# Kernel optimization log

Hardware: AMD Instinct MI355X
Metric: run time of the kernel (lower is better)

## Reference

```python
import jax, jax.numpy as jnp
import numpy as np

N_NODES = 50000
N_EDGES = 800000
IN_DIM = 128
HID = 128
N_LAYERS = 2


def setup_inputs() -> dict:
    key = jax.random.key(0)
    ks = jax.random.split(key, 16)
    x = jax.random.normal(ks[0], (N_NODES, IN_DIM), dtype=jnp.float32)
    edge_index = jax.random.randint(ks[1], (2, N_EDGES), 0, N_NODES, dtype=jnp.int64)
    def lin(k, fan_in, fan_out):
        bound = 1.0 / np.sqrt(fan_in)
        k1, k2 = jax.random.split(k)
        W = jax.random.uniform(k1, (fan_in, fan_out), jnp.float32, -bound, bound)
        b = jax.random.uniform(k2, (fan_out,), jnp.float32, -bound, bound)
        return W, b
    W1_0, b1_0 = lin(ks[2], IN_DIM, HID)
    W2_0, b2_0 = lin(ks[3], HID, HID)
    W1_1, b1_1 = lin(ks[4], HID, HID)
    W2_1, b2_1 = lin(ks[5], HID, HID)
    Wr, br = lin(ks[6], HID, 1)
    return dict(x=x, edge_index=edge_index,
                W1_0=W1_0, b1_0=b1_0, W2_0=W2_0, b2_0=b2_0,
                W1_1=W1_1, b1_1=b1_1, W2_1=W2_1, b2_1=b2_1,
                Wr=Wr, br=br)


def _gin_conv(x, src, dst, W1, b1, W2, b2):
    # GINConv (eps=0): h = MLP(x + sum_{j in N(i)} x_j)
    msgs = x[src]                                   # [E, d] gather
    agg = jax.ops.segment_sum(msgs, dst, num_segments=x.shape[0])  # [N, d] scatter-add
    h = x + agg
    h = jax.nn.relu(h @ W1 + b1)
    return h @ W2 + b2


def reference(x, edge_index, W1_0, b1_0, W2_0, b2_0, W1_1, b1_1, W2_1, b2_1, Wr, br):
    src, dst = edge_index[0], edge_index[1]
    # layer 0
    h = jax.nn.relu(_gin_conv(x, src, dst, W1_0, b1_0, W2_0, b2_0))
    # layer 1 (dropout is identity in eval mode)
    h = jax.nn.relu(_gin_conv(h, src, dst, W1_1, b1_1, W2_1, b2_1))
    return h @ Wr + br
```

## Files before the change

kernel.cpp:

```cpp
#include <hip/hip_runtime.h>

#define HIDDEN 128
#define NB_SHIFT 7
#define NPB 128
#define EPB 4096

typedef __attribute__((ext_vector_type(8))) short short8;
typedef __attribute__((ext_vector_type(4))) float f32x4;
typedef _Float16 f16;
typedef __attribute__((ext_vector_type(8))) _Float16 f16x8;

__device__ __forceinline__ ushort f2bf(float a) {
  union { float f; unsigned u; } c; c.f = a;
  return (ushort)((c.u + 0x7FFFu + ((c.u >> 16) & 1u)) >> 16);
}
__device__ __forceinline__ float bf2f(ushort h) {
  union { unsigned u; float f; } c; c.u = ((unsigned)h) << 16;
  return c.f;
}

__global__ __launch_bounds__(256) void bucket_hist_kernel(
    const int* __restrict__ dst, int* __restrict__ bcnt, int E, int NB) {
  __shared__ int loc[512];
  const int t = threadIdx.x;
  loc[t] = 0; loc[t + 256] = 0;
  __syncthreads();
  const int base = blockIdx.x * EPB;
  const int end = min(base + EPB, E);
  for (int e = base + t; e < end; e += 256)
    atomicAdd(&loc[dst[e] >> NB_SHIFT], 1);
  __syncthreads();
  for (int b = t; b < NB; b += 256)
    if (loc[b]) atomicAdd(&bcnt[b], loc[b]);
}

__global__ __launch_bounds__(256) void scan_buckets_kernel(
    const int* __restrict__ bcnt, int* __restrict__ pairOff,
    int* __restrict__ gCursor, int NB) {
  __shared__ int sh[512];
  const int t = threadIdx.x;
  const int v0 = (t < NB) ? bcnt[t] : 0;
  const int v1 = (t + 256 < NB) ? bcnt[t + 256] : 0;
  sh[t] = v0; sh[t + 256] = v1;
  __syncthreads();
#pragma unroll
  for (int off = 1; off < 512; off <<= 1) {
    int a = (t >= off) ? sh[t - off] : 0;
    int b = (t + 256 >= off) ? sh[t + 256 - off] : 0;
    __syncthreads();
    sh[t] += a; sh[t + 256] += b;
    __syncthreads();
  }
  const int e0 = sh[t] - v0;
  const int e1 = sh[t + 256] - v1;
  pairOff[t] = e0; gCursor[t] = e0;
  pairOff[t + 256] = e1; gCursor[t + 256] = e1;
  if (t == 255) pairOff[512] = sh[511];
}

__global__ __launch_bounds__(256) void partition_kernel(
    const int* __restrict__ src, const int* __restrict__ dst,
    int* __restrict__ gCursor, int* __restrict__ pairs, int E, int NB) {
  __shared__ int loc[512];
  __shared__ int cur[512];
  const int t = threadIdx.x;
  loc[t] = 0; loc[t + 256] = 0;
  __syncthreads();
  const int base = blockIdx.x * EPB;
  const int end = min(base + EPB, E);
  for (int e = base + t; e < end; e += 256)
    atomicAdd(&loc[dst[e] >> NB_SHIFT], 1);
  __syncthreads();
  for (int b = t; b < NB; b += 256)
    cur[b] = loc[b] ? atomicAdd(&gCursor[b], loc[b]) : 0;
  __syncthreads();
  for (int e = base + t; e < end; e += 256) {
    const int d = dst[e];
    const int p = atomicAdd(&cur[d >> NB_SHIFT], 1);
    pairs[p] = ((d & (NPB - 1)) << 25) | src[e];
  }
}

__global__ __launch_bounds__(256) void build_csr_kernel(
    const int* __restrict__ pairs, const int* __restrict__ pairOff,
    int* __restrict__ rowptr, int* __restrict__ col, int M, int E, int NB) {
  __shared__ int deg[NPB];
  __shared__ int pre[NPB];
  __shared__ int cur[NPB];
  const int b = blockIdx.x;
  const int t = threadIdx.x;
  const int s = pairOff[b];
  const int e2 = pairOff[b + 1];
  const int nodeBase = b << NB_SHIFT;
  const int nNodes = min(NPB, M - nodeBase);
  if (t < NPB) deg[t] = 0;
  __syncthreads();
  for (int i = s + t; i < e2; i += 256)
    atomicAdd(&deg[((unsigned)pairs[i]) >> 25], 1);
  __syncthreads();
  if (t < NPB) pre[t] = deg[t];
  __syncthreads();
#pragma unroll
  for (int off = 1; off < NPB; off <<= 1) {
    int v = (t < NPB && t >= off) ? pre[t - off] : 0;
    __syncthreads();
    if (t < NPB) pre[t] += v;
    __syncthreads();
  }
  if (t < nNodes) rowptr[nodeBase + t] = s + pre[t] - deg[t];
  if (b == NB - 1 && t == 0) rowptr[M] = E;
  if (t < NPB) cur[t] = pre[t] - deg[t];
  __syncthreads();
  for (int i = s + t; i < e2; i += 256) {
    const int pr = pairs[i];
    const int pos = s + atomicAdd(&cur[((unsigned)pr) >> 25], 1);
    col[pos] = pr & 0x1FFFFFF;
  }
}

__global__ __launch_bounds__(256) void f2h_kernel(const float* __restrict__ in,
                                                  f16* __restrict__ out, int n8) {
  int i = blockIdx.x * 256 + threadIdx.x;
  if (i >= n8) return;
  const float4* p = (const float4*)(in + (size_t)i * 8);
  float4 a = p[0], b = p[1];
  f16x8 o;
  o[0] = (f16)a.x; o[1] = (f16)a.y; o[2] = (f16)a.z; o[3] = (f16)a.w;
  o[4] = (f16)b.x; o[5] = (f16)b.y; o[6] = (f16)b.z; o[7] = (f16)b.w;
  *(f16x8*)(out + (size_t)i * 8) = o;
}

__global__ __launch_bounds__(256) void prepack_kernel(
    const float* __restrict__ Wa, const float* __restrict__ Wb,
    const float* __restrict__ Wc, const float* __restrict__ Wd,
    ushort* __restrict__ out) {
  int idx = blockIdx.x * 256 + threadIdx.x;
  int w = idx >> 11;
  int rem = idx & 2047;
  int ks = rem >> 9;
  int nf = (rem >> 6) & 7;
  int lane = rem & 63;
  const float* W = (w == 0) ? Wa : (w == 1) ? Wb : (w == 2) ? Wc : Wd;
  const int kbase = ks * 32 + (lane >> 4) * 8;
  const int n = nf * 16 + (lane & 15);
  ushort* oh = out + (size_t)w * 32768 + (size_t)rem * 8;
  ushort* ol = oh + 16384;
#pragma unroll
  for (int j = 0; j < 8; ++j) {
    float v = W[(size_t)(kbase + j) * HIDDEN + n];
    ushort h = f2bf(v);
    oh[j] = h;
    ol[j] = f2bf(v - bf2f(h));
  }
}

__global__ __launch_bounds__(256, 4) void gin_layer_kernel(
    const f16* __restrict__ xh, const int* __restrict__ rowptr,
    const int* __restrict__ col, const ushort* __restrict__ W1p,
    const float* __restrict__ b1, const ushort* __restrict__ W2p,
    const float* __restrict__ b2, f16* __restrict__ Ch,
    const float* __restrict__ Wr, const float* __restrict__ br,
    float* __restrict__ outv, int M, int doReadout) {
  __shared__ float h1[4][16][132];
  const int t = threadIdx.x;
  const int lane = t & 63;
  const int w = t >> 6;
  const int r = lane & 15;
  const int g = lane >> 4;
  const int mBase = blockIdx.x * 64 + w * 16;
  int arow = mBase + r;
  if (arow > M - 1) arow = M - 1;

  float a32[4][8];
  {
    const f16* rp = xh + (size_t)arow * HIDDEN + g * 8;
    f16x8 s0 = *(const f16x8*)(rp);
    f16x8 s1 = *(const f16x8*)(rp + 32);
    f16x8 s2 = *(const f16x8*)(rp + 64);
    f16x8 s3 = *(const f16x8*)(rp + 96);
#pragma unroll
    for (int j = 0; j < 8; ++j) {
      a32[0][j] = (float)s0[j]; a32[1][j] = (float)s1[j];
      a32[2][j] = (float)s2[j]; a32[3][j] = (float)s3[j];
    }
    const int s = rowptr[arow];
    const int e = rowptr[arow + 1];
    int i = s;
    for (; i + 1 < e; i += 2) {
      const int c0 = col[i], c1 = col[i + 1];
      const f16* p0 = xh + (size_t)c0 * HIDDEN + g * 8;
      const f16* p1 = xh + (size_t)c1 * HIDDEN + g * 8;
      f16x8 u0 = *(const f16x8*)(p0);
      f16x8 u1 = *(const f16x8*)(p0 + 32);
      f16x8 u2 = *(const f16x8*)(p0 + 64);
      f16x8 u3 = *(const f16x8*)(p0 + 96);
      f16x8 v0 = *(const f16x8*)(p1);
      f16x8 v1 = *(const f16x8*)(p1 + 32);
      f16x8 v2 = *(const f16x8*)(p1 + 64);
      f16x8 v3 = *(const f16x8*)(p1 + 96);
#pragma unroll
      for (int j = 0; j < 8; ++j) {
        a32[0][j] += (float)u0[j] + (float)v0[j];
        a32[1][j] += (float)u1[j] + (float)v1[j];
        a32[2][j] += (float)u2[j] + (float)v2[j];
        a32[3][j] += (float)u3[j] + (float)v3[j];
      }
    }
    if (i < e) {
      const int c0 = col[i];
      const f16* p0 = xh + (size_t)c0 * HIDDEN + g * 8;
      f16x8 u0 = *(const f16x8*)(p0);
      f16x8 u1 = *(const f16x8*)(p0 + 32);
      f16x8 u2 = *(const f16x8*)(p0 + 64);
      f16x8 u3 = *(const f16x8*)(p0 + 96);
#pragma unroll
      for (int j = 0; j < 8; ++j) {
        a32[0][j] += (float)u0[j];
        a32[1][j] += (float)u1[j];
        a32[2][j] += (float)u2[j];
        a32[3][j] += (float)u3[j];
      }
    }
  }

  f32x4 acc[8];
#pragma unroll
  for (int i = 0; i < 8; ++i) acc[i] = (f32x4){0.f, 0.f, 0.f, 0.f};

#pragma unroll
  for (int ks = 0; ks < 4; ++ks) {
    short8 ah, al;
#pragma unroll
    for (int j = 0; j < 8; ++j) {
      ushort h = f2bf(a32[ks][j]);
      ah[j] = (short)h;
      al[j] = (short)f2bf(a32[ks][j] - bf2f(h));
    }
#pragma unroll
    for (int nf = 0; nf < 8; ++nf) {
      const ushort* bp = W1p + ((size_t)(ks * 8 + nf) * 64 + lane) * 8;
      short8 bh = *(const short8*)bp;
      short8 bl = *(const short8*)(bp + 16384);
      acc[nf] = __builtin_amdgcn_mfma_f32_16x16x32_bf16(ah, bh, acc[nf], 0, 0, 0);
      acc[nf] = __builtin_amdgcn_mfma_f32_16x16x32_bf16(al, bh, acc[nf], 0, 0, 0);
      acc[nf] = __builtin_amdgcn_mfma_f32_16x16x32_bf16(ah, bl, acc[nf], 0, 0, 0);
    }
  }

#pragma unroll
  for (int nf = 0; nf < 8; ++nf) {
    float bv = b1[nf * 16 + r];
#pragma unroll
    for (int q = 0; q < 4; ++q)
      h1[w][g * 4 + q][nf * 16 + r] = fmaxf(acc[nf][q] + bv, 0.f);
    acc[nf] = (f32x4){0.f, 0.f, 0.f, 0.f};
  }

#pragma unroll
  for (int ks = 0; ks < 4; ++ks) {
    const float* hp = &h1[w][r][ks * 32 + g * 8];
    float4 a0 = *(const float4*)hp;
    float4 a1 = *(const float4*)(hp + 4);
    float av[8] = {a0.x, a0.y, a0.z, a0.w, a1.x, a1.y, a1.z, a1.w};
    short8 ah, al;
#pragma unroll
    for (int j = 0; j < 8; ++j) {
      ushort h = f2bf(av[j]);
      ah[j] = (short)h;
      al[j] = (short)f2bf(av[j] - bf2f(h));
    }
#pragma unroll
    for (int nf = 0; nf < 8; ++nf) {
      const ushort* bp = W2p + ((size_t)(ks * 8 + nf) * 64 + lane) * 8;
      short8 bh = *(const short8*)bp;
      short8 bl = *(const short8*)(bp + 16384);
      acc[nf] = __builtin_amdgcn_mfma_f32_16x16x32_bf16(ah, bh, acc[nf], 0, 0, 0);
      acc[nf] = __builtin_amdgcn_mfma_f32_16x16x32_bf16(al, bh, acc[nf], 0, 0, 0);
      acc[nf] = __builtin_amdgcn_mfma_f32_16x16x32_bf16(ah, bl, acc[nf], 0, 0, 0);
    }
  }

  if (!doReadout) {
#pragma unroll
    for (int nf = 0; nf < 8; ++nf) {
      float bv = b2[nf * 16 + r];
#pragma unroll
      for (int q = 0; q < 4; ++q)
        h1[w][g * 4 + q][nf * 16 + r] = fmaxf(acc[nf][q] + bv, 0.f);
    }
    const int rr = lane >> 2;
    const int c0 = (lane & 3) * 32;
    const int gm = blockIdx.x * 64 + w * 16 + rr;
    if (gm < M) {
#pragma unroll
      for (int i = 0; i < 4; ++i) {
        float4 v0 = *(const float4*)&h1[w][rr][c0 + i * 8];
        float4 v1 = *(const float4*)&h1[w][rr][c0 + i * 8 + 4];
        f16x8 o;
        o[0] = (f16)v0.x; o[1] = (f16)v0.y; o[2] = (f16)v0.z; o[3] = (f16)v0.w;
        o[4] = (f16)v1.x; o[5] = (f16)v1.y; o[6] = (f16)v1.z; o[7] = (f16)v1.w;
        *(f16x8*)(Ch + (size_t)gm * HIDDEN + c0 + i * 8) = o;
      }
    }
  } else {
    float p[4] = {0.f, 0.f, 0.f, 0.f};
#pragma unroll
    for (int nf = 0; nf < 8; ++nf) {
      float bv = b2[nf * 16 + r];
      float wv = Wr[nf * 16 + r];
#pragma unroll
      for (int q = 0; q < 4; ++q) {
        float h = fmaxf(acc[nf][q] + bv, 0.f);
        p[q] += h * wv;
      }
    }
#pragma unroll
    for (int q = 0; q < 4; ++q) {
      p[q] += __shfl_xor(p[q], 8);
      p[q] += __shfl_xor(p[q], 4);
      p[q] += __shfl_xor(p[q], 2);
      p[q] += __shfl_xor(p[q], 1);
    }
    if (r == 0) {
      float brv = br[0];
#pragma unroll
      for (int q = 0; q < 4; ++q) {
        int gm = mBase + g * 4 + q;
        if (gm < M) outv[gm] = p[q] + brv;
      }
    }
  }
}

extern "C" void kernel_launch(void* const* d_in, const int* in_sizes, int n_in,
                              void* d_out, int out_size, void* d_ws,
                              size_t ws_size, hipStream_t stream) {
  const float* x = (const float*)d_in[0];
  const int* ei = (const int*)d_in[1];
  const float* W1_0 = (const float*)d_in[2];
  const float* b1_0 = (const float*)d_in[3];
  const float* W2_0 = (const float*)d_in[4];
  const float* b2_0 = (const float*)d_in[5];
  const float* W1_1 = (const float*)d_in[6];
  const float* b1_1 = (const float*)d_in[7];
  const float* W2_1 = (const float*)d_in[8];
  const float* b2_1 = (const float*)d_in[9];
  const float* Wr = (const float*)d_in[10];
  const float* br = (const float*)d_in[11];

  const int M = in_sizes[0] / HIDDEN;
  const int E = in_sizes[1] / 2;
  const int* src = ei;
  const int* dst = ei + E;
  const int NB = (M + NPB - 1) >> NB_SHIFT;

  int* pairs = (int*)d_ws;
  f16* xh = (f16*)(pairs + E);
  f16* Bh = xh + (size_t)M * HIDDEN;
  int* rowptr = (int*)(Bh + (size_t)M * HIDDEN);
  int* col = rowptr + M + 1;
  int* bcnt = col + E;
  int* pairOff = bcnt + 512;
  int* gCursor = pairOff + 513;
  ushort* Wpk = (ushort*)(gCursor + 512);

  const int mlpBlocks = (M + 63) / 64;
  const int cvtBlocks = (M * 16 + 255) / 256;
  const int edgeBlocks = (E + EPB - 1) / EPB;
  float* out = (float*)d_out;

  prepack_kernel<<<32, 256, 0, stream>>>(W1_0, W2_0, W1_1, W2_1, Wpk);
  f2h_kernel<<<cvtBlocks, 256, 0, stream>>>(x, xh, M * 16);

  hipMemsetAsync(bcnt, 0, 512 * sizeof(int), stream);
  bucket_hist_kernel<<<edgeBlocks, 256, 0, stream>>>(dst, bcnt, E, NB);
  scan_buckets_kernel<<<1, 256, 0, stream>>>(bcnt, pairOff, gCursor, NB);
  partition_kernel<<<edgeBlocks, 256, 0, stream>>>(src, dst, gCursor, pairs,
                                                   E, NB);
  build_csr_kernel<<<NB, 256, 0, stream>>>(pairs, pairOff, rowptr, col, M, E,
                                           NB);

  gin_layer_kernel<<<mlpBlocks, 256, 0, stream>>>(
      xh, rowptr, col, Wpk, b1_0, Wpk + 32768, b2_0, Bh,
      nullptr, nullptr, nullptr, M, 0);

  gin_layer_kernel<<<mlpBlocks, 256, 0, stream>>>(
      Bh, rowptr, col, Wpk + 65536, b1_1, Wpk + 98304, b2_1, nullptr,
      Wr, br, out, M, 1);
}
```

Before: 254.1 us.

## Gather neighbors with warp-per-row coalesced loads staged through shared memory

Restructures the aggregation so each wavefront handles 16 rows sequentially, with each lane owning two feature columns. Each neighbor row is then read as one contiguous 256-byte access across the wave instead of 16 scattered rows per wave, and the column indices are batched eight at a time with masking. The aggregated rows go through shared memory to build the MFMA A fragments. Blocks shrink to 128 threads covering 32 rows. Rows are processed serially within a wave, which limits memory-level parallelism per wave and adds a shared-memory round trip.

```diff
diff --git a/kernel.cpp b/kernel.cpp
--- a/kernel.cpp
+++ b/kernel.cpp
@@ -8,6 +8,7 @@
 typedef __attribute__((ext_vector_type(8))) short short8;
 typedef __attribute__((ext_vector_type(4))) float f32x4;
 typedef _Float16 f16;
+typedef __attribute__((ext_vector_type(2))) _Float16 f16x2;
 typedef __attribute__((ext_vector_type(8))) _Float16 f16x8;
 
 __device__ __forceinline__ ushort f2bf(float a) {
@@ -154,87 +155,67 @@
   }
 }
 
-__global__ __launch_bounds__(256, 4) void gin_layer_kernel(
+__global__ __launch_bounds__(128, 4) void gin_layer_kernel(
     const f16* __restrict__ xh, const int* __restrict__ rowptr,
     const int* __restrict__ col, const ushort* __restrict__ W1p,
     const float* __restrict__ b1, const ushort* __restrict__ W2p,
     const float* __restrict__ b2, f16* __restrict__ Ch,
     const float* __restrict__ Wr, const float* __restrict__ br,
     float* __restrict__ outv, int M, int doReadout) {
-  __shared__ float h1[4][16][132];
+  __shared__ float h1[2][16][133];
   const int t = threadIdx.x;
   const int lane = t & 63;
   const int w = t >> 6;
   const int r = lane & 15;
   const int g = lane >> 4;
-  const int mBase = blockIdx.x * 64 + w * 16;
-  int arow = mBase + r;
-  if (arow > M - 1) arow = M - 1;
-
-  float a32[4][8];
-  {
-    const f16* rp = xh + (size_t)arow * HIDDEN + g * 8;
-    f16x8 s0 = *(const f16x8*)(rp);
-    f16x8 s1 = *(const f16x8*)(rp + 32);
-    f16x8 s2 = *(const f16x8*)(rp + 64);
-    f16x8 s3 = *(const f16x8*)(rp + 96);
+  const int mBase = blockIdx.x * 32 + w * 16;
+  const int d0 = lane * 2;
+
+  for (int n = 0; n < 16; ++n) {
+    int row = mBase + n;
+    if (row > M - 1) row = M - 1;
+    const int s = rowptr[row];
+    const int e = rowptr[row + 1];
+    f16x2 sv = *(const f16x2*)(xh + (size_t)row * HIDDEN + d0);
+    float ax = (float)sv.x, ay = (float)sv.y;
+    for (int i = s; i < e; i += 8) {
+      int cc[8];
+#pragma unroll
+      for (int j = 0; j < 8; ++j) {
+        int idx = i + j;
+        cc[j] = col[idx < e ? idx : e - 1];
+      }
+      f16x2 v[8];
+#pragma unroll
+      for (int j = 0; j < 8; ++j)
+        v[j] = *(const f16x2*)(xh + (size_t)cc[j] * HIDDEN + d0);
+#pragma unroll
+      for (int j = 0; j < 8; ++j) {
+        const bool ok = (i + j) < e;
+        ax += ok ? (float)v[j].x : 0.f;
+        ay += ok ? (float)v[j].y : 0.f;
+      }
+    }
+    h1[w][n][d0] = ax;
+    h1[w][n][d0 + 1] = ay;
+  }
+
+  f32x4 acc[8];
+#pragma unroll
+  for (int i = 0; i < 8; ++i) acc[i] = (f32x4){0.f, 0.f, 0.f, 0.f};
+
+#pragma unroll
+  for (int ks = 0; ks < 4; ++ks) {
+    const float* hp = &h1[w][r][ks * 32 + g * 8];
+    float4 a0 = *(const float4*)hp;
+    float4 a1 = *(const float4*)(hp + 4);
+    float av[8] = {a0.x, a0.y, a0.z, a0.w, a1.x, a1.y, a1.z, a1.w};
+    short8 ah, al;
 #pragma unroll
     for (int j = 0; j < 8; ++j) {
-      a32[0][j] = (float)s0[j]; a32[1][j] = (float)s1[j];
-      a32[2][j] = (float)s2[j]; a32[3][j] = (float)s3[j];
-    }
-    const int s = rowptr[arow];
-    const int e = rowptr[arow + 1];
-    int i = s;
-    for (; i + 1 < e; i += 2) {
-      const int c0 = col[i], c1 = col[i + 1];
-      const f16* p0 = xh + (size_t)c0 * HIDDEN + g * 8;
-      const f16* p1 = xh + (size_t)c1 * HIDDEN + g * 8;
-      f16x8 u0 = *(const f16x8*)(p0);
-      f16x8 u1 = *(const f16x8*)(p0 + 32);
-      f16x8 u2 = *(const f16x8*)(p0 + 64);
-      f16x8 u3 = *(const f16x8*)(p0 + 96);
-      f16x8 v0 = *(const f16x8*)(p1);
-      f16x8 v1 = *(const f16x8*)(p1 + 32);
-      f16x8 v2 = *(const f16x8*)(p1 + 64);
-      f16x8 v3 = *(const f16x8*)(p1 + 96);
-#pragma unroll
-      for (int j = 0; j < 8; ++j) {
-        a32[0][j] += (float)u0[j] + (float)v0[j];
-        a32[1][j] += (float)u1[j] + (float)v1[j];
-        a32[2][j] += (float)u2[j] + (float)v2[j];
-        a32[3][j] += (float)u3[j] + (float)v3[j];
-      }
-    }
-    if (i < e) {
-      const int c0 = col[i];
-      const f16* p0 = xh + (size_t)c0 * HIDDEN + g * 8;
-      f16x8 u0 = *(const f16x8*)(p0);
-      f16x8 u1 = *(const f16x8*)(p0 + 32);
-      f16x8 u2 = *(const f16x8*)(p0 + 64);
-      f16x8 u3 = *(const f16x8*)(p0 + 96);
-#pragma unroll
-      for (int j = 0; j < 8; ++j) {
-        a32[0][j] += (float)u0[j];
-        a32[1][j] += (float)u1[j];
-        a32[2][j] += (float)u2[j];
-        a32[3][j] += (float)u3[j];
-      }
-    }
-  }
-
-  f32x4 acc[8];
-#pragma unroll
-  for (int i = 0; i < 8; ++i) acc[i] = (f32x4){0.f, 0.f, 0.f, 0.f};
-
-#pragma unroll
-  for (int ks = 0; ks < 4; ++ks) {
-    short8 ah, al;
-#pragma unroll
-    for (int j = 0; j < 8; ++j) {
-      ushort h = f2bf(a32[ks][j]);
+      ushort h = f2bf(av[j]);
       ah[j] = (short)h;
-      al[j] = (short)f2bf(a32[ks][j] - bf2f(h));
+      al[j] = (short)f2bf(av[j] - bf2f(h));
     }
 #pragma unroll
     for (int nf = 0; nf < 8; ++nf) {
@@ -290,7 +271,7 @@
     }
     const int rr = lane >> 2;
     const int c0 = (lane & 3) * 32;
-    const int gm = blockIdx.x * 64 + w * 16 + rr;
+    const int gm = mBase + rr;
     if (gm < M) {
 #pragma unroll
       for (int i = 0; i < 4; ++i) {
@@ -364,7 +345,7 @@
   int* gCursor = pairOff + 513;
   ushort* Wpk = (ushort*)(gCursor + 512);
 
-  const int mlpBlocks = (M + 63) / 64;
+  const int ginBlocks = (M + 31) / 32;
   const int cvtBlocks = (M * 16 + 255) / 256;
   const int edgeBlocks = (E + EPB - 1) / EPB;
   float* out = (float*)d_out;
@@ -380,11 +361,11 @@
   build_csr_kernel<<<NB, 256, 0, stream>>>(pairs, pairOff, rowptr, col, M, E,
                                            NB);
 
-  gin_layer_kernel<<<mlpBlocks, 256, 0, stream>>>(
+  gin_layer_kernel<<<ginBlocks, 128, 0, stream>>>(
       xh, rowptr, col, Wpk, b1_0, Wpk + 32768, b2_0, Bh,
       nullptr, nullptr, nullptr, M, 0);
 
-  gin_layer_kernel<<<mlpBlocks, 256, 0, stream>>>(
+  gin_layer_kernel<<<ginBlocks, 128, 0, stream>>>(
       Bh, rowptr, col, Wpk + 65536, b1_1, Wpk + 98304, b2_1, nullptr,
       Wr, br, out, M, 1);
 }
```

Result: slower. 282.1 us (+11.0%).

## Sort nodes by degree to balance per-wavefront aggregation work

Applied to the files above, without the earlier changes.

Adds a counting sort of nodes by in-degree (histogram, descending scan, scatter) that builds a permutation. Both GIN layer kernels then process rows in permuted order and write results back through it, so lanes in a wavefront gather neighbour lists of similar length and less divergence is wasted. The cost is three extra small launches, an indirection load per row, and scattered output writes. The LDS padding also changes from 132 to 133.

```diff
diff --git a/kernel.cpp b/kernel.cpp
--- a/kernel.cpp
+++ b/kernel.cpp
@@ -116,6 +116,48 @@
     const int pos = s + atomicAdd(&cur[((unsigned)pr) >> 25], 1);
     col[pos] = pr & 0x1FFFFFF;
   }
+}
+
+__global__ __launch_bounds__(256) void deg_hist_kernel(
+    const int* __restrict__ rowptr, int* __restrict__ dhist, int M) {
+  __shared__ int loc[256];
+  const int t = threadIdx.x;
+  loc[t] = 0;
+  __syncthreads();
+  const int n = blockIdx.x * 256 + t;
+  if (n < M) {
+    int d = rowptr[n + 1] - rowptr[n];
+    atomicAdd(&loc[min(d, 255)], 1);
+  }
+  __syncthreads();
+  if (loc[t]) atomicAdd(&dhist[t], loc[t]);
+}
+
+__global__ __launch_bounds__(256) void deg_scan_kernel(
+    const int* __restrict__ dhist, int* __restrict__ dcur) {
+  __shared__ int sh[256];
+  const int t = threadIdx.x;
+  const int v = dhist[255 - t];
+  sh[t] = v;
+  __syncthreads();
+#pragma unroll
+  for (int off = 1; off < 256; off <<= 1) {
+    int a = (t >= off) ? sh[t - off] : 0;
+    __syncthreads();
+    sh[t] += a;
+    __syncthreads();
+  }
+  dcur[255 - t] = sh[t] - v;
+}
+
+__global__ __launch_bounds__(256) void deg_scatter_kernel(
+    const int* __restrict__ rowptr, int* __restrict__ dcur,
+    int* __restrict__ perm, int M) {
+  const int n = blockIdx.x * 256 + threadIdx.x;
+  if (n >= M) return;
+  const int d = min(rowptr[n + 1] - rowptr[n], 255);
+  const int pos = atomicAdd(&dcur[d], 1);
+  perm[pos] = n;
 }
 
 __global__ __launch_bounds__(256) void f2h_kernel(const float* __restrict__ in,
@@ -156,20 +198,22 @@
 
 __global__ __launch_bounds__(256, 4) void gin_layer_kernel(
     const f16* __restrict__ xh, const int* __restrict__ rowptr,
-    const int* __restrict__ col, const ushort* __restrict__ W1p,
-    const float* __restrict__ b1, const ushort* __restrict__ W2p,
-    const float* __restrict__ b2, f16* __restrict__ Ch,
-    const float* __restrict__ Wr, const float* __restrict__ br,
-    float* __restrict__ outv, int M, int doReadout) {
-  __shared__ float h1[4][16][132];
+    const int* __restrict__ col, const int* __restrict__ perm,
+    const ushort* __restrict__ W1p, const float* __restrict__ b1,
+    const ushort* __restrict__ W2p, const float* __restrict__ b2,
+    f16* __restrict__ Ch, const float* __restrict__ Wr,
+    const float* __restrict__ br, float* __restrict__ outv, int M,
+    int doReadout) {
+  __shared__ float h1[4][16][133];
   const int t = threadIdx.x;
   const int lane = t & 63;
   const int w = t >> 6;
   const int r = lane & 15;
   const int g = lane >> 4;
   const int mBase = blockIdx.x * 64 + w * 16;
-  int arow = mBase + r;
-  if (arow > M - 1) arow = M - 1;
+  int lrow = mBase + r;
+  if (lrow > M - 1) lrow = M - 1;
+  const int arow = perm[lrow];
 
   float a32[4][8];
   {
@@ -290,8 +334,9 @@
     }
     const int rr = lane >> 2;
     const int c0 = (lane & 3) * 32;
-    const int gm = blockIdx.x * 64 + w * 16 + rr;
+    const int gm = mBase + rr;
     if (gm < M) {
+      const int orow = perm[gm];
 #pragma unroll
       for (int i = 0; i < 4; ++i) {
         float4 v0 = *(const float4*)&h1[w][rr][c0 + i * 8];
@@ -299,7 +344,7 @@
         f16x8 o;
         o[0] = (f16)v0.x; o[1] = (f16)v0.y; o[2] = (f16)v0.z; o[3] = (f16)v0.w;
         o[4] = (f16)v1.x; o[5] = (f16)v1.y; o[6] = (f16)v1.z; o[7] = (f16)v1.w;
-        *(f16x8*)(Ch + (size_t)gm * HIDDEN + c0 + i * 8) = o;
+        *(f16x8*)(Ch + (size_t)orow * HIDDEN + c0 + i * 8) = o;
       }
     }
   } else {
@@ -326,7 +371,7 @@
 #pragma unroll
       for (int q = 0; q < 4; ++q) {
         int gm = mBase + g * 4 + q;
-        if (gm < M) outv[gm] = p[q] + brv;
+        if (gm < M) outv[perm[gm]] = p[q] + brv;
       }
     }
   }
@@ -362,17 +407,22 @@
   int* bcnt = col + E;
   int* pairOff = bcnt + 512;
   int* gCursor = pairOff + 513;
-  ushort* Wpk = (ushort*)(gCursor + 512);
-
-  const int mlpBlocks = (M + 63) / 64;
+  int* dhist = gCursor + 512;
+  int* dcur = dhist + 256;
+  int* perm = dcur + 256;
+  ushort* Wpk = (ushort*)(perm + M);
+
+  const int ginBlocks = (M + 63) / 64;
   const int cvtBlocks = (M * 16 + 255) / 256;
   const int edgeBlocks = (E + EPB - 1) / EPB;
+  const int nodeBlocks = (M + 255) / 256;
   float* out = (float*)d_out;
 
   prepack_kernel<<<32, 256, 0, stream>>>(W1_0, W2_0, W1_1, W2_1, Wpk);
   f2h_kernel<<<cvtBlocks, 256, 0, stream>>>(x, xh, M * 16);
 
   hipMemsetAsync(bcnt, 0, 512 * sizeof(int), stream);
+  hipMemsetAsync(dhist, 0, 256 * sizeof(int), stream);
   bucket_hist_kernel<<<edgeBlocks, 256, 0, stream>>>(dst, bcnt, E, NB);
   scan_buckets_kernel<<<1, 256, 0, stream>>>(bcnt, pairOff, gCursor, NB);
   partition_kernel<<<edgeBlocks, 256, 0, stream>>>(src, dst, gCursor, pairs,
@@ -380,11 +430,15 @@
   build_csr_kernel<<<NB, 256, 0, stream>>>(pairs, pairOff, rowptr, col, M, E,
                                            NB);
 
-  gin_layer_kernel<<<mlpBlocks, 256, 0, stream>>>(
-      xh, rowptr, col, Wpk, b1_0, Wpk + 32768, b2_0, Bh,
+  deg_hist_kernel<<<nodeBlocks, 256, 0, stream>>>(rowptr, dhist, M);
+  deg_scan_kernel<<<1, 256, 0, stream>>>(dhist, dcur);
+  deg_scatter_kernel<<<nodeBlocks, 256, 0, stream>>>(rowptr, dcur, perm, M);
+
+  gin_layer_kernel<<<ginBlocks, 256, 0, stream>>>(
+      xh, rowptr, col, perm, Wpk, b1_0, Wpk + 32768, b2_0, Bh,
       nullptr, nullptr, nullptr, M, 0);
 
-  gin_layer_kernel<<<mlpBlocks, 256, 0, stream>>>(
-      Bh, rowptr, col, Wpk + 65536, b1_1, Wpk + 98304, b2_1, nullptr,
+  gin_layer_kernel<<<ginBlocks, 256, 0, stream>>>(
+      Bh, rowptr, col, perm, Wpk + 65536, b1_1, Wpk + 98304, b2_1, nullptr,
       Wr, br, out, M, 1);
 }
```

New measurement: 399.6 us. 57.2% more time.
